# Kernel tuning notes

Hardware: AMD Instinct MI355X
Metric: run time of the kernel (lower is better)

## Reference

```python
import jax, jax.numpy as jnp
import numpy as np

V = 50257  # vocab_size
L = 4096   # sequence length (unbatched)
H1 = 30    # emb / lstm1 hidden
H2 = 50    # lstm2 hidden


def setup_inputs() -> dict:
    key = jax.random.key(0)
    ks = jax.random.split(key, 14)
    init = lambda k, sh: (jax.random.normal(k, sh, jnp.float32) * 0.05)
    return {
        "x": jax.random.randint(ks[0], (L,), 0, V),
        "emb": init(ks[1], (V, H1)),
        "w_ih1": init(ks[2], (4 * H1, H1)),
        "w_hh1": init(ks[3], (4 * H1, H1)),
        "b_ih1": init(ks[4], (4 * H1,)),
        "b_hh1": init(ks[5], (4 * H1,)),
        "w1": init(ks[6], (H2, H1)),
        "bl1": init(ks[7], (H2,)),
        "w_ih2": init(ks[8], (4 * H2, H2)),
        "w_hh2": init(ks[9], (4 * H2, H2)),
        "b_ih2": init(ks[10], (4 * H2,)),
        "b_hh2": init(ks[11], (4 * H2,)),
        "w2": init(ks[12], (V, H2)),
        "bl2": init(ks[13], (V,)),
    }


def _lstm(x, w_ih, w_hh, b_ih, b_hh):
    """PyTorch-semantics single-layer LSTM over [L, H_in], zero init state.
    Gate order i, f, g, o. Returns hidden states [L, H]."""
    H = w_hh.shape[1]
    # precompute the input contribution for all timesteps: [L, 4H]
    gx = x @ w_ih.T + b_ih + b_hh

    def step(carry, g_t):
        h, c = carry
        g = g_t + h @ w_hh.T
        i, f, gg, o = jnp.split(g, 4)
        c = jax.nn.sigmoid(f) * c + jax.nn.sigmoid(i) * jnp.tanh(gg)
        h = jax.nn.sigmoid(o) * jnp.tanh(c)
        return (h, c), h

    z = jnp.zeros((H,), x.dtype)
    _, hs = jax.lax.scan(step, (z, z), gx)
    return hs


def reference(x, emb, w_ih1, w_hh1, b_ih1, b_hh1, w1, bl1,
              w_ih2, w_hh2, b_ih2, b_hh2, w2, bl2):
    h = emb[x]                                   # [L, 30]
    h = _lstm(h, w_ih1, w_hh1, b_ih1, b_hh1)     # [L, 30]
    h = h @ w1.T + bl1                           # [L, 50]
    h = _lstm(h, w_ih2, w_hh2, b_ih2, b_hh2)     # [L, 50]
    return h @ w2.T + bl2                        # [L, V]
```

## Files before the change

### kernel.cpp

```cpp
#include <hip/hip_runtime.h>
#include <hip/hip_bf16.h>

#define V 50257
#define L 4096
#define H1 30
#define H2 50
#define G1N 120
#define G2N 200

#define OFF_WIH1 16
#define OFF_WHH1 (OFF_WIH1 + G1N*H1)
#define OFF_B1   (OFF_WHH1 + G1N*H1)
#define OFF_WC   (OFF_B1 + G1N)
#define OFF_BC   (OFF_WC + G2N*H1)
#define OFF_WHH2 (OFF_BC + G2N)
#define OFF_GX1  (OFF_WHH2 + G2N*H2)
#define OFF_H2   (OFF_GX1 + L*G1N)

__device__ __forceinline__ float fast_rcp(float x){
#if __has_builtin(__builtin_amdgcn_rcpf)
  return __builtin_amdgcn_rcpf(x);
#else
  return 1.f/x;
#endif
}
__device__ __forceinline__ float sigf(float x){
  return fast_rcp(1.f + __expf(-x));
}
__device__ __forceinline__ float tanh_f(float x){
  return 2.f*sigf(2.f*x) - 1.f;
}

template<int BF>
__device__ __forceinline__ float ldN(const void* p, long i){
  if (BF) return __bfloat162float(((const __hip_bfloat16*)p)[i]);
  return ((const float*)p)[i];
}
__device__ __forceinline__ float ldF(const void* p, long i, int bf){
  return bf ? __bfloat162float(((const __hip_bfloat16*)p)[i])
            : ((const float*)p)[i];
}

__global__ void k_detect(const unsigned* emb, int* flag){
  __shared__ int cnt;
  if (threadIdx.x == 0) cnt = 0;
  __syncthreads();
  unsigned w = emb[threadIdx.x];
  unsigned e = (w >> 7) & 0xffu;
  int hit = (e >= 90u && e <= 130u) ? 1 : 0;
  atomicAdd(&cnt, hit);
  __syncthreads();
  if (threadIdx.x == 0) *flag = (cnt >= 192) ? 1 : 0;
}

__global__ void k_prep(float* ws, const void* w_ih1, const void* w_hh1,
                       const void* b_ih1, const void* b_hh1,
                       const void* w1, const void* bl1,
                       const void* w_ih2, const void* w_hh2,
                       const void* b_ih2, const void* b_hh2){
  int bf = ((const int*)ws)[0];
  int gid = blockIdx.x*blockDim.x + threadIdx.x;
  int gsz = gridDim.x*blockDim.x;
  for (int i=gid; i<G1N*H1; i+=gsz) ws[OFF_WIH1+i] = ldF(w_ih1,i,bf);
  for (int i=gid; i<G1N*H1; i+=gsz) ws[OFF_WHH1+i] = ldF(w_hh1,i,bf);
  for (int i=gid; i<G1N;    i+=gsz) ws[OFF_B1+i]   = ldF(b_ih1,i,bf)+ldF(b_hh1,i,bf);
  for (int i=gid; i<G2N*H2; i+=gsz) ws[OFF_WHH2+i] = ldF(w_hh2,i,bf);
  for (int i=gid; i<G2N; i+=gsz){
    float a = ldF(b_ih2,i,bf) + ldF(b_hh2,i,bf);
    for (int k=0;k<H2;k++) a += ldF(w_ih2,(long)i*H2+k,bf)*ldF(bl1,k,bf);
    ws[OFF_BC+i] = a;
  }
  for (int i=gid; i<G2N*H1; i+=gsz){
    int o = i / H1, j = i % H1;
    float a = 0.f;
    for (int k=0;k<H2;k++) a += ldF(w_ih2,(long)o*H2+k,bf)*ldF(w1,(long)k*H1+j,bf);
    ws[OFF_WC+i] = a;
  }
}

__global__ void k_embed(const int* __restrict__ x, const void* __restrict__ emb,
                        float* __restrict__ ws){
  int bf = ((const int*)ws)[0];
  __shared__ float er[2][H1];
  int half = threadIdx.x >> 7;
  int lane = threadIdx.x & 127;
  int t = blockIdx.x*2 + half;
  int idx = x[t];
  if (lane < H1) er[half][lane] = ldF(emb,(long)idx*H1+lane,bf);
  __syncthreads();
  if (lane < G1N){
    const float* wi = ws + OFF_WIH1 + lane*H1;
    float a = ws[OFF_B1 + lane];
    #pragma unroll
    for (int k=0;k<H1;k++) a += er[half][k]*wi[k];
    ws[OFF_GX1 + (long)t*G1N + lane] = a;
  }
}

__global__ __launch_bounds__(384) void k_recur(float* __restrict__ ws){
  const float* whh1 = ws + OFF_WHH1;
  const float* wcm  = ws + OFF_WC;
  const float* bcm  = ws + OFF_BC;
  const float* whh2 = ws + OFF_WHH2;
  const float* gx1  = ws + OFF_GX1;
  float* h2o = ws + OFF_H2;

  __shared__ __align__(16) float h1s[32];
  __shared__ __align__(16) float h2s[52];
  __shared__ float g1s[G1N];
  __shared__ float g2s[G2N];

  int tid = threadIdx.x;
  bool g1l = (tid < G1N);
  bool g2l = (tid >= 128) && (tid < 128 + G2N);
  int o2 = tid - 128;

  float w[84];
  #pragma unroll
  for (int k=0;k<84;k++) w[k] = 0.f;
  float bcv = 0.f;
  if (g1l){
    #pragma unroll
    for (int k=0;k<H1;k++) w[k] = whh1[tid*H1+k];
  } else if (g2l){
    #pragma unroll
    for (int k=0;k<H1;k++) w[k] = wcm[o2*H1+k];
    #pragma unroll
    for (int k=0;k<H2;k++) w[32+k] = whh2[o2*H2+k];
    bcv = bcm[o2];
  }
  bool u1l = (tid < H1);
  bool u2l = (tid >= 64) && (tid < 64 + H2);
  int j2 = tid - 64;
  float c1 = 0.f, c2 = 0.f;
  if (tid < 32) h1s[tid] = 0.f;
  if (tid < 52) h2s[tid] = 0.f;
  __syncthreads();

  float gv = g1l ? gx1[tid] : 0.f;
  for (int t=0; t<=L; ++t){
    float gvn = (g1l && (t+1 < L)) ? gx1[(long)(t+1)*G1N + tid] : 0.f;

    if (g1l && t < L){
      float a0=gv, a1=0.f, a2=0.f, a3=0.f;
      const float4* hp = (const float4*)h1s;
      #pragma unroll
      for (int i=0;i<8;i++){
        float4 h4 = hp[i];
        a0 += w[4*i+0]*h4.x; a1 += w[4*i+1]*h4.y;
        a2 += w[4*i+2]*h4.z; a3 += w[4*i+3]*h4.w;
      }
      g1s[tid] = (a0+a1)+(a2+a3);
    }
    if (g2l && t >= 1){
      float a0=bcv, a1=0.f, a2=0.f, a3=0.f;
      const float4* hp = (const float4*)h1s;
      #pragma unroll
      for (int i=0;i<8;i++){
        float4 h4 = hp[i];
        a0 += w[4*i+0]*h4.x; a1 += w[4*i+1]*h4.y;
        a2 += w[4*i+2]*h4.z; a3 += w[4*i+3]*h4.w;
      }
      const float4* hq = (const float4*)h2s;
      #pragma unroll
      for (int i=0;i<13;i++){
        float4 h4 = hq[i];
        a0 += w[32+4*i+0]*h4.x; a1 += w[32+4*i+1]*h4.y;
        a2 += w[32+4*i+2]*h4.z; a3 += w[32+4*i+3]*h4.w;
      }
      g2s[o2] = (a0+a1)+(a2+a3);
    }
    __syncthreads();

    if (u1l && t < L){
      float gi=g1s[tid], gf=g1s[H1+tid], gg=g1s[2*H1+tid], go=g1s[3*H1+tid];
      c1 = sigf(gf)*c1 + sigf(gi)*tanh_f(gg);
      h1s[tid] = sigf(go)*tanh_f(c1);
    }
    if (u2l && t >= 1){
      float gi=g2s[j2], gf=g2s[H2+j2], gg=g2s[2*H2+j2], go=g2s[3*H2+j2];
      c2 = sigf(gf)*c2 + sigf(gi)*tanh_f(gg);
      float h = sigf(go)*tanh_f(c2);
      h2s[j2] = h;
      h2o[(long)(t-1)*H2 + j2] = h;
    }
    __syncthreads();
    gv = gvn;
  }
}

template<int BF>
__device__ void gemm_body(const float* __restrict__ ws, const void* __restrict__ w2,
                          const void* __restrict__ bl2, void* __restrict__ outv){
  const float* __restrict__ h2 = ws + OFF_H2;
  int c  = blockIdx.x*512 + threadIdx.x*2;
  int r0 = blockIdx.y*128;
  long ca = (c   < V) ? c   : (V-1);
  long cb = (c+1 < V) ? c+1 : (V-1);
  float wa[H2], wb[H2];
  #pragma unroll
  for (int k=0;k<H2;k++){ wa[k]=ldN<BF>(w2, ca*H2+k); wb[k]=ldN<BF>(w2, cb*H2+k); }
  float bav = ldN<BF>(bl2, ca), bbv = ldN<BF>(bl2, cb);
  bool va = (c < V), vb = (c+1 < V);
  for (int r=r0; r<r0+128; ++r){
    const float* __restrict__ h = h2 + (long)r*H2;
    float a0=bav, a1=0.f, b0=bbv, b1=0.f;
    #pragma unroll
    for (int k=0;k<H2;k+=2){
      float h0=h[k], h1v=h[k+1];
      a0 += h0*wa[k];   a1 += h1v*wa[k+1];
      b0 += h0*wb[k];   b1 += h1v*wb[k+1];
    }
    float ra = a0+a1, rb = b0+b1;
    long base = (long)r*V;
    if (BF){
      __hip_bfloat16* o = (__hip_bfloat16*)outv;
      if (va) o[base+c]   = __float2bfloat16(ra);
      if (vb) o[base+c+1] = __float2bfloat16(rb);
    } else {
      float* o = (float*)outv;
      if (va) o[base+c]   = ra;
      if (vb) o[base+c+1] = rb;
    }
  }
}

__global__ __launch_bounds__(256) void k_gemm(const float* __restrict__ ws,
                                              const void* __restrict__ w2,
                                              const void* __restrict__ bl2,
                                              void* __restrict__ outv){
  if (((const int*)ws)[0]) gemm_body<1>(ws, w2, bl2, outv);
  else                     gemm_body<0>(ws, w2, bl2, outv);
}

extern "C" void kernel_launch(void* const* d_in, const int* in_sizes, int n_in,
                              void* d_out, int out_size, void* d_ws, size_t ws_size,
                              hipStream_t stream){
  const int* x = (const int*)d_in[0];
  const void* emb = d_in[1];
  float* ws = (float*)d_ws;

  k_detect<<<1, 256, 0, stream>>>((const unsigned*)emb, (int*)d_ws);
  k_prep<<<64, 256, 0, stream>>>(ws, d_in[2], d_in[3], d_in[4], d_in[5],
                                 d_in[6], d_in[7], d_in[8], d_in[9],
                                 d_in[10], d_in[11]);
  k_embed<<<L/2, 256, 0, stream>>>(x, emb, ws);
  k_recur<<<1, 384, 0, stream>>>(ws);
  dim3 g((V + 511)/512, L/128);
  k_gemm<<<g, 256, 0, stream>>>(ws, d_in[12], d_in[13], d_out);
}
```

Baseline: 4.565 ms.

## Gather LSTM gates via lane shuffles and double-buffer hidden state to drop a barrier

The gate rows are reordered so that the four gates (i,f,g,o) of each hidden unit sit in four adjacent lanes. The gates are combined with xor-shuffles, and every lane computes the cell update redundantly. The hidden state is double-buffered in shared memory, which removes the gate shared-memory round-trip and one of the two __syncthreads per timestep in the serial recurrence. The embed kernel writes gx1 in the matching permuted layout. In exchange, the cell math is repeated four times per unit, which puts more ALU work on the critical path.

Result: faster. 4.454 ms (-2.5%).

```diff
diff --git a/kernel.cpp b/kernel.cpp
--- a/kernel.cpp
+++ b/kernel.cpp
@@ -29,6 +29,31 @@
 }
 __device__ __forceinline__ float tanh_f(float x){
   return 2.f*sigf(2.f*x) - 1.f;
+}
+
+__device__ __forceinline__ float dot4(float4 a, float4 b){
+  return a.x*b.x + a.y*b.y + a.z*b.z + a.w*b.w;
+}
+__device__ __forceinline__ float4 ld4(const float* r){
+  return float4{r[0], r[1], r[2], r[3]};
+}
+__device__ __forceinline__ float4 ld2z(const float* r){
+  return float4{r[0], r[1], 0.f, 0.f};
+}
+
+__device__ __forceinline__ void gather4(float a, int q,
+                                        float& gi, float& gf, float& gg, float& go){
+  float t1 = __shfl_xor(a, 1);
+  float u1 = __shfl_xor(a, 2);
+  float v1 = __shfl_xor(t1, 2);
+  float e0 = (q&1) ? t1 : a;
+  float e1 = (q&1) ? a  : t1;
+  float f0 = (q&1) ? v1 : u1;
+  float f1 = (q&1) ? u1 : v1;
+  gi = (q&2) ? f0 : e0;
+  gf = (q&2) ? f1 : e1;
+  gg = (q&2) ? e0 : f0;
+  go = (q&2) ? e1 : f1;
 }
 
 template<int BF>
@@ -93,7 +118,8 @@
     float a = ws[OFF_B1 + lane];
     #pragma unroll
     for (int k=0;k<H1;k++) a += er[half][k]*wi[k];
-    ws[OFF_GX1 + (long)t*G1N + lane] = a;
+    int pi = 4*(lane % 30) + lane / 30;
+    ws[OFF_GX1 + (long)t*G1N + pi] = a;
   }
 }
 
@@ -105,87 +131,102 @@
   const float* gx1  = ws + OFF_GX1;
   float* h2o = ws + OFF_H2;
 
-  __shared__ __align__(16) float h1s[32];
-  __shared__ __align__(16) float h2s[52];
-  __shared__ float g1s[G1N];
-  __shared__ float g2s[G2N];
+  __shared__ __align__(16) float hb1[2][32];
+  __shared__ __align__(16) float hb2[2][52];
 
   int tid = threadIdx.x;
   bool g1l = (tid < G1N);
   bool g2l = (tid >= 128) && (tid < 128 + G2N);
-  int o2 = tid - 128;
-
-  float w[84];
-  #pragma unroll
-  for (int k=0;k<84;k++) w[k] = 0.f;
+  int rel = tid - 128;
+  int q1 = tid & 3,  j1 = tid >> 2;
+  int q2 = rel & 3,  k2 = rel >> 2;
+
+  float4 w0{0,0,0,0}, w1{0,0,0,0}, w2{0,0,0,0}, w3{0,0,0,0};
+  float4 w4{0,0,0,0}, w5{0,0,0,0}, w6{0,0,0,0}, w7{0,0,0,0};
+  float4 v0{0,0,0,0}, v1{0,0,0,0}, v2{0,0,0,0}, v3{0,0,0,0};
+  float4 v4{0,0,0,0}, v5{0,0,0,0}, v6{0,0,0,0}, v7{0,0,0,0};
+  float4 v8{0,0,0,0}, v9{0,0,0,0}, v10{0,0,0,0}, v11{0,0,0,0}, v12{0,0,0,0};
   float bcv = 0.f;
+
   if (g1l){
-    #pragma unroll
-    for (int k=0;k<H1;k++) w[k] = whh1[tid*H1+k];
+    const float* r = whh1 + (30*q1 + j1)*H1;
+    w0=ld4(r); w1=ld4(r+4); w2=ld4(r+8); w3=ld4(r+12);
+    w4=ld4(r+16); w5=ld4(r+20); w6=ld4(r+24); w7=ld2z(r+28);
   } else if (g2l){
-    #pragma unroll
-    for (int k=0;k<H1;k++) w[k] = wcm[o2*H1+k];
-    #pragma unroll
-    for (int k=0;k<H2;k++) w[32+k] = whh2[o2*H2+k];
-    bcv = bcm[o2];
-  }
-  bool u1l = (tid < H1);
-  bool u2l = (tid >= 64) && (tid < 64 + H2);
-  int j2 = tid - 64;
+    int row = 50*q2 + k2;
+    const float* r  = wcm  + row*H1;
+    const float* r2 = whh2 + row*H2;
+    w0=ld4(r); w1=ld4(r+4); w2=ld4(r+8); w3=ld4(r+12);
+    w4=ld4(r+16); w5=ld4(r+20); w6=ld4(r+24); w7=ld2z(r+28);
+    v0=ld4(r2); v1=ld4(r2+4); v2=ld4(r2+8); v3=ld4(r2+12);
+    v4=ld4(r2+16); v5=ld4(r2+20); v6=ld4(r2+24); v7=ld4(r2+28);
+    v8=ld4(r2+32); v9=ld4(r2+36); v10=ld4(r2+40); v11=ld4(r2+44);
+    v12=ld2z(r2+48);
+    bcv = bcm[row];
+  }
+
   float c1 = 0.f, c2 = 0.f;
-  if (tid < 32) h1s[tid] = 0.f;
-  if (tid < 52) h2s[tid] = 0.f;
+  {
+    float* f1 = (float*)hb1;
+    float* f2 = (float*)hb2;
+    if (tid < 64)  f1[tid] = 0.f;
+    if (tid < 104) f2[tid] = 0.f;
+  }
   __syncthreads();
 
   float gv = g1l ? gx1[tid] : 0.f;
+  int p = 0;
   for (int t=0; t<=L; ++t){
     float gvn = (g1l && (t+1 < L)) ? gx1[(long)(t+1)*G1N + tid] : 0.f;
+    const float* h1r = hb1[p];
+    const float* h2r = hb2[p];
+    float* h1w = hb1[p^1];
+    float* h2w = hb2[p^1];
 
     if (g1l && t < L){
-      float a0=gv, a1=0.f, a2=0.f, a3=0.f;
-      const float4* hp = (const float4*)h1s;
-      #pragma unroll
-      for (int i=0;i<8;i++){
-        float4 h4 = hp[i];
-        a0 += w[4*i+0]*h4.x; a1 += w[4*i+1]*h4.y;
-        a2 += w[4*i+2]*h4.z; a3 += w[4*i+3]*h4.w;
-      }
-      g1s[tid] = (a0+a1)+(a2+a3);
+      const float4* hp = (const float4*)h1r;
+      float4 x0=hp[0], x1=hp[1], x2=hp[2], x3=hp[3];
+      float4 x4=hp[4], x5=hp[5], x6=hp[6], x7=hp[7];
+      float a0 = gv + dot4(w0,x0) + dot4(w4,x4);
+      float a1 =      dot4(w1,x1) + dot4(w5,x5);
+      float a2 =      dot4(w2,x2) + dot4(w6,x6);
+      float a3 =      dot4(w3,x3) + dot4(w7,x7);
+      float gval = (a0+a1)+(a2+a3);
+      float gi,gf,gg,go;
+      gather4(gval, q1, gi, gf, gg, go);
+      c1 = sigf(gf)*c1 + sigf(gi)*tanh_f(gg);
+      float h = sigf(go)*tanh_f(c1);
+      if (q1 == 0) h1w[j1] = h;
     }
     if (g2l && t >= 1){
-      float a0=bcv, a1=0.f, a2=0.f, a3=0.f;
-      const float4* hp = (const float4*)h1s;
-      #pragma unroll
-      for (int i=0;i<8;i++){
-        float4 h4 = hp[i];
-        a0 += w[4*i+0]*h4.x; a1 += w[4*i+1]*h4.y;
-        a2 += w[4*i+2]*h4.z; a3 += w[4*i+3]*h4.w;
-      }
-      const float4* hq = (const float4*)h2s;
-      #pragma unroll
-      for (int i=0;i<13;i++){
-        float4 h4 = hq[i];
-        a0 += w[32+4*i+0]*h4.x; a1 += w[32+4*i+1]*h4.y;
-        a2 += w[32+4*i+2]*h4.z; a3 += w[32+4*i+3]*h4.w;
-      }
-      g2s[o2] = (a0+a1)+(a2+a3);
-    }
-    __syncthreads();
-
-    if (u1l && t < L){
-      float gi=g1s[tid], gf=g1s[H1+tid], gg=g1s[2*H1+tid], go=g1s[3*H1+tid];
-      c1 = sigf(gf)*c1 + sigf(gi)*tanh_f(gg);
-      h1s[tid] = sigf(go)*tanh_f(c1);
-    }
-    if (u2l && t >= 1){
-      float gi=g2s[j2], gf=g2s[H2+j2], gg=g2s[2*H2+j2], go=g2s[3*H2+j2];
+      const float4* hp = (const float4*)h1r;
+      const float4* hq = (const float4*)h2r;
+      float4 x0=hp[0], x1=hp[1], x2=hp[2], x3=hp[3];
+      float4 x4=hp[4], x5=hp[5], x6=hp[6], x7=hp[7];
+      float4 y0=hq[0], y1=hq[1], y2=hq[2], y3=hq[3];
+      float4 y4=hq[4], y5=hq[5], y6=hq[6], y7=hq[7];
+      float4 y8=hq[8], y9=hq[9], y10=hq[10], y11=hq[11], y12=hq[12];
+      float a0 = bcv + dot4(w0,x0) + dot4(w4,x4)
+                     + dot4(v0,y0) + dot4(v4,y4) + dot4(v8,y8) + dot4(v12,y12);
+      float a1 =       dot4(w1,x1) + dot4(w5,x5)
+                     + dot4(v1,y1) + dot4(v5,y5) + dot4(v9,y9);
+      float a2 =       dot4(w2,x2) + dot4(w6,x6)
+                     + dot4(v2,y2) + dot4(v6,y6) + dot4(v10,y10);
+      float a3 =       dot4(w3,x3) + dot4(w7,x7)
+                     + dot4(v3,y3) + dot4(v7,y7) + dot4(v11,y11);
+      float gval = (a0+a1)+(a2+a3);
+      float gi,gf,gg,go;
+      gather4(gval, q2, gi, gf, gg, go);
       c2 = sigf(gf)*c2 + sigf(gi)*tanh_f(gg);
       float h = sigf(go)*tanh_f(c2);
-      h2s[j2] = h;
-      h2o[(long)(t-1)*H2 + j2] = h;
+      if (q2 == 0){
+        h2w[k2] = h;
+        h2o[(long)(t-1)*H2 + k2] = h;
+      }
     }
     __syncthreads();
     gv = gvn;
+    p ^= 1;
   }
 }
 
```
